# Performance work log

Hardware: AMD Instinct MI355X
Metric: run time of the kernel (lower is better)

Reference implementation:

```python
import jax, jax.numpy as jnp
import numpy as np

HEADS = 32
K_TOP = 512  # top-k tokens gathered from KV


def conv3d(x, w, b=None, pad=0, groups=1):
    # x: [B,C,D,H,W], w: [O, I/groups, kd,kh,kw]
    out = jax.lax.conv_general_dilated(
        x, w, window_strides=(1, 1, 1), padding=[(pad, pad)] * 3,
        dimension_numbers=("NCDHW", "OIDHW", "NCDHW"), feature_group_count=groups)
    if b is not None:
        out = out + b[None, :, None, None, None]
    return out


def setup_inputs() -> dict:
    key = jax.random.key(0)
    ks = jax.random.split(key, 10)
    B, C, D, H, W = 2, 256, 16, 16, 16
    p = lambda i, shape: (jax.random.normal(ks[i], shape, jnp.float32) * 0.02)
    return {
        "x_kv": jax.random.normal(ks[0], (B, C, D, H, W), jnp.float32),
        "x_q": jax.random.normal(ks[1], (B, C, D, H, W), jnp.float32),
        "w_spa": p(2, (1, 2, 7, 7, 7)),            # SpatialAttention conv, no bias
        "w_kv": p(3, (C, 2 * C)), "b_kv": jnp.zeros((2 * C,), jnp.float32),
        "w_q": p(4, (C, C)), "b_q": jnp.zeros((C,), jnp.float32),
        "w_proj": p(5, (C, C)), "b_proj": jnp.zeros((C,), jnp.float32),
        "w_dw": p(6, (C, 1, 3, 3, 3)), "b_dw": jnp.zeros((C,), jnp.float32),  # depthwise 3x3x3
        "w_pw": p(7, (C, C, 1, 1, 1)), "b_pw": jnp.zeros((C,), jnp.float32),  # pointwise 1x1x1
    }


def reference(x_kv, x_q, w_spa, w_kv, b_kv, w_q, b_q, w_proj, b_proj,
              w_dw, b_dw, w_pw, b_pw):
    B, C, D, H, W = x_kv.shape
    N = D * H * W
    hd = C // HEADS
    scale = hd ** -0.5

    # SpatialAttention: channel mean/max -> conv(2->1, k=7, pad=3) -> sigmoid
    avg = jnp.mean(x_kv, axis=1, keepdims=True)
    mx = jnp.max(x_kv, axis=1, keepdims=True)
    spa = jax.nn.sigmoid(conv3d(jnp.concatenate([avg, mx], axis=1), w_spa, None, pad=3))
    scores = spa.reshape(B, N)                      # [B, N]
    _, idx = jax.lax.top_k(scores, K_TOP)           # [B, K] (descending, like torch.topk)

    # Full K/V projection over all N tokens (as in original), then gather top-k
    xkv_t = x_kv.reshape(B, C, N).transpose(0, 2, 1)        # [B, N, C]
    kv = xkv_t @ w_kv + b_kv                                 # [B, N, 2C]
    k_full, v_full = kv[..., :C], kv[..., C:]
    k_g = jnp.take_along_axis(k_full, idx[:, :, None], axis=1)  # [B, K, C]
    v_g = jnp.take_along_axis(v_full, idx[:, :, None], axis=1)
    k_g = k_g.reshape(B, K_TOP, HEADS, hd).transpose(0, 2, 1, 3)  # [B, h, K, d]
    v_g = v_g.reshape(B, K_TOP, HEADS, hd).transpose(0, 2, 1, 3)

    # Queries over all Nq tokens
    xq_t = x_q.reshape(B, C, N).transpose(0, 2, 1)           # [B, N, C]
    q = (xq_t @ w_q + b_q).reshape(B, N, HEADS, hd).transpose(0, 2, 1, 3)  # [B, h, N, d]

    attn = jax.nn.softmax(jnp.einsum('bhnd,bhkd->bhnk', q, k_g) * scale, axis=-1)
    out = jnp.einsum('bhnk,bhkd->bhnd', attn, v_g)           # [B, h, N, d]
    out = out.transpose(0, 2, 1, 3).reshape(B, N, C)
    out = out @ w_proj + b_proj
    out = out.transpose(0, 2, 1).reshape(B, C, D, H, W)

    # DWconv residual on full (ungathered) V
    v_vol = v_full.transpose(0, 2, 1).reshape(B, C, D, H, W)
    res = conv3d(conv3d(v_vol, w_dw, b_dw, pad=1, groups=C), w_pw, b_pw)
    return out + res
```

## Files before the change

### kernel.cpp

```cpp
#include <hip/hip_runtime.h>
#include <hip/hip_bf16.h>

typedef short bf16x8 __attribute__((ext_vector_type(8)));
typedef float f32x4 __attribute__((ext_vector_type(4)));

constexpr int CN = 256, NV = 4096, KTOP = 512;

static __device__ __forceinline__ unsigned short f2bf(float f) {
  __hip_bfloat16 h = __float2bfloat16(f);
  return *(unsigned short*)&h;
}
static __device__ __forceinline__ unsigned pack2(float a, float b) {
  return (unsigned)f2bf(a) | ((unsigned)f2bf(b) << 16);
}
static __device__ __forceinline__ float bf2f(unsigned short u) {
  return __uint_as_float(((unsigned)u) << 16);
}
static __device__ __forceinline__ unsigned packtrunc(float a, float b) {
  return (__float_as_uint(a) >> 16) | (__float_as_uint(b) & 0xFFFF0000u);
}

__global__ void __launch_bounds__(256) k_tcast2(const float* __restrict__ srcA,
                                                const float* __restrict__ srcB,
                                                unsigned short* __restrict__ dstA,
                                                unsigned short* __restrict__ dstB,
                                                float* __restrict__ avgmx) {
  __shared__ float tile[64 * 65];
  int z = blockIdx.z;
  int t = threadIdx.x;
  if (z == 4) {
    __shared__ float ssum[256], smax[256];
    int blk = blockIdx.y * 64 + blockIdx.x;
    int b = blk >> 7, n0 = (blk & 127) * 32;
    int cg = t >> 5, nl = t & 31;
    int n = n0 + nl;
    const float* p = srcA + (size_t)b * CN * NV + (size_t)cg * 32 * NV + n;
    float s = 0.f, m = -1e30f;
    for (int i = 0; i < 32; ++i) {
      float v = p[(size_t)i * NV];
      s += v; m = fmaxf(m, v);
    }
    ssum[t] = s; smax[t] = m;
    __syncthreads();
    if (cg == 0) {
      for (int g = 1; g < 8; ++g) { s += ssum[g * 32 + nl]; m = fmaxf(m, smax[g * 32 + nl]); }
      avgmx[(b * 2 + 0) * NV + n] = s * (1.0f / 256.0f);
      avgmx[(b * 2 + 1) * NV + n] = m;
    }
    return;
  }
  int b = z & 1;
  const float* s = (z < 2 ? srcA : srcB) + (size_t)b * CN * NV;
  unsigned short* d = (z < 2 ? dstA : dstB) + (size_t)b * NV * 256;
  int c0 = blockIdx.y * 64, n0 = blockIdx.x * 64;
  for (int i = 0; i < 16; ++i) {
    int id = i * 256 + t, c = id >> 6, n = id & 63;
    tile[c * 65 + n] = s[(size_t)(c0 + c) * NV + n0 + n];
  }
  __syncthreads();
  int n = t & 63, part = t >> 6;
  unsigned w[8];
#pragma unroll
  for (int k = 0; k < 8; ++k)
    w[k] = pack2(tile[(part * 16 + 2 * k) * 65 + n], tile[(part * 16 + 2 * k + 1) * 65 + n]);
  uint4* p = (uint4*)&d[(size_t)(n0 + n) * 256 + c0 + part * 16];
  p[0] = make_uint4(w[0], w[1], w[2], w[3]);
  p[1] = make_uint4(w[4], w[5], w[6], w[7]);
}

__global__ void __launch_bounds__(256) k_wprep(const float* __restrict__ wkv,
                                               const float* __restrict__ wq,
                                               const float* __restrict__ wproj,
                                               const float* __restrict__ wpw,
                                               unsigned short* __restrict__ wv_t,
                                               unsigned short* __restrict__ wq_t,
                                               unsigned short* __restrict__ wcat,
                                               unsigned short* __restrict__ wk_t) {
  __shared__ float tile[64 * 65];
  int role = blockIdx.z;
  int j0 = blockIdx.x * 64, c0 = blockIdx.y * 64;
  int t = threadIdx.x;
  if (role == 3) {
    int j = t >> 2, part = t & 3;
    const float* s = &wpw[(size_t)(j0 + j) * 256 + c0 + part * 16];
    unsigned w[8];
#pragma unroll
    for (int k = 0; k < 8; ++k) w[k] = pack2(s[2 * k], s[2 * k + 1]);
    uint4* p = (uint4*)&wcat[(size_t)(j0 + j) * 512 + 256 + c0 + part * 16];
    p[0] = make_uint4(w[0], w[1], w[2], w[3]);
    p[1] = make_uint4(w[4], w[5], w[6], w[7]);
    return;
  }
  const float* src; int srcLD, srcOff; unsigned short* dst; int dstLD;
  if (role == 0)      { src = wkv;   srcLD = 512; srcOff = 256; dst = wv_t; dstLD = 256; }
  else if (role == 1) { src = wq;    srcLD = 256; srcOff = 0;   dst = wq_t; dstLD = 256; }
  else if (role == 4) { src = wkv;   srcLD = 512; srcOff = 0;   dst = wk_t; dstLD = 256; }
  else                { src = wproj; srcLD = 256; srcOff = 0;   dst = wcat; dstLD = 512; }
  for (int i = 0; i < 16; ++i) {
    int id = i * 256 + t, c = id >> 6, j = id & 63;
    tile[c * 65 + j] = src[(size_t)(c0 + c) * srcLD + srcOff + j0 + j];
  }
  __syncthreads();
  int j = t & 63, part = t >> 6;
  unsigned w[8];
#pragma unroll
  for (int k = 0; k < 8; ++k)
    w[k] = pack2(tile[(part * 16 + 2 * k) * 65 + j], tile[(part * 16 + 2 * k + 1) * 65 + j]);
  uint4* p = (uint4*)&dst[(size_t)(j0 + j) * dstLD + c0 + part * 16];
  p[0] = make_uint4(w[0], w[1], w[2], w[3]);
  p[1] = make_uint4(w[4], w[5], w[6], w[7]);
}

__global__ void __launch_bounds__(256) k_spa(const float* __restrict__ avgmx,
                                             const float* __restrict__ wspa,
                                             float* __restrict__ scores) {
  __shared__ float vol[2 * 4096];
  __shared__ float ws[686];
  int b = blockIdx.x >> 5, chunk = blockIdx.x & 31;
  int tid = threadIdx.x;
  for (int t = tid; t < 8192; t += 256) vol[t] = avgmx[b * 8192 + t];
  for (int t = tid; t < 686; t += 256) ws[t] = wspa[t];
  __syncthreads();
  int ci = tid & 1;
  int n = chunk * 128 + (tid >> 1);
  int d = n >> 8, h = (n >> 4) & 15, w = n & 15;
  const float* vb = vol + ci * 4096;
  const float* wb = ws + ci * 343;
  float acc = 0.f;
  for (int kd = 0; kd < 7; ++kd) {
    int zd = d - 3 + kd; if ((unsigned)zd >= 16u) continue;
    for (int kh = 0; kh < 7; ++kh) {
      int zh = h - 3 + kh; if ((unsigned)zh >= 16u) continue;
      const float* row = vb + zd * 256 + zh * 16;
      const float* wr = wb + kd * 49 + kh * 7;
#pragma unroll
      for (int kw = 0; kw < 7; ++kw) {
        int zw = w - 3 + kw;
        if ((unsigned)zw < 16u) acc += row[zw] * wr[kw];
      }
    }
  }
  acc += __shfl_xor(acc, 1);
  if (ci == 0) scores[b * NV + n] = 1.0f / (1.0f + expf(-acc));
}

__global__ void __launch_bounds__(1024) k_topk(const float* __restrict__ scores,
                                               int* __restrict__ idx) {
  __shared__ unsigned sv[4096];
  __shared__ int sB;
  __shared__ unsigned sSub, scnt;
  __shared__ unsigned hist[256];
  __shared__ int wsum[16];
  int b = blockIdx.x, tid = threadIdx.x;
  for (int t = tid; t < 4096; t += 1024) sv[t] = __float_as_uint(scores[b * NV + t]);
  if (tid == 0) scnt = 0;
  unsigned prefix = 0;
  int r = 512;
  for (int shift = 24; shift >= 0; shift -= 8) {
    if (tid < 256) hist[tid] = 0;
    __syncthreads();
    unsigned maskhi = (shift == 24) ? 0u : (0xFFFFFFFFu << (shift + 8));
    for (int i = 0; i < 4; ++i) {
      unsigned v = sv[tid + i * 1024];
      if ((v & maskhi) == prefix) atomicAdd(&hist[(v >> shift) & 255], 1u);
    }
    __syncthreads();
    if (tid < 64) {
      int lane = tid;
      unsigned h0 = hist[lane * 4 + 0], h1 = hist[lane * 4 + 1];
      unsigned h2 = hist[lane * 4 + 2], h3 = hist[lane * 4 + 3];
      unsigned s = h0 + h1 + h2 + h3;
      for (int off = 1; off < 64; off <<= 1) {
        unsigned y = __shfl_down(s, off);
        if (lane + off < 64) s += y;
      }
      unsigned tail = __shfl_down(s, 1);
      if (lane == 63) tail = 0;
      unsigned s3 = tail + h3, s2 = s3 + h2, s1 = s2 + h1, s0 = s1 + h0;
      unsigned sx[5] = {s0, s1, s2, s3, tail};
#pragma unroll
      for (int i = 0; i < 4; ++i)
        if (sx[i] >= (unsigned)r && sx[i + 1] < (unsigned)r) { sB = lane * 4 + i; sSub = sx[i + 1]; }
    }
    __syncthreads();
    prefix |= ((unsigned)sB) << shift;
    r -= (int)sSub;
    __syncthreads();
  }
  unsigned vstar = prefix;
  for (int i = 0; i < 4; ++i) {
    int t = tid * 4 + i;
    if (sv[t] > vstar) { unsigned p = atomicAdd(&scnt, 1u); idx[b * KTOP + p] = t; }
  }
  __syncthreads();
  int base = (int)scnt;
  int loc = 0;
  for (int i = 0; i < 4; ++i) loc += (sv[tid * 4 + i] == vstar);
  int lane = tid & 63, w = tid >> 6;
  int x = loc;
  for (int off = 1; off < 64; off <<= 1) {
    int y = __shfl_up(x, off);
    if (lane >= off) x += y;
  }
  if (lane == 63) wsum[w] = x;
  __syncthreads();
  int wbase = 0;
  for (int i = 0; i < w; ++i) wbase += wsum[i];
  int excl = wbase + x - loc;
  for (int i = 0; i < 4; ++i) {
    int t = tid * 4 + i;
    if (sv[t] == vstar) {
      if (excl < r) idx[b * KTOP + base + excl] = t;
      ++excl;
    }
  }
}

__global__ void __launch_bounds__(256) k_qv(const unsigned short* __restrict__ xkv_t,
                                            const unsigned short* __restrict__ xq_t,
                                            const unsigned short* __restrict__ wv_t,
                                            const unsigned short* __restrict__ wq_t,
                                            const float* __restrict__ bkv,
                                            const float* __restrict__ bq,
                                            unsigned short* __restrict__ v_nc,
                                            unsigned short* __restrict__ qh) {
  __shared__ unsigned short Als[128 * 40];
  __shared__ unsigned short Bls[128 * 40];
  int role = blockIdx.z;
  int b = role & 1;
  bool isQ = role >= 2;
  const unsigned short* A = isQ ? wq_t : wv_t;
  const unsigned short* B = (isQ ? xq_t : xkv_t) + (size_t)b * NV * 256;
  const float* bias = isQ ? bq : (bkv + 256);
  int n0 = blockIdx.x * 128, j0 = blockIdx.y * 128;
  int t = threadIdx.x;
  int wave = t >> 6, lane = t & 63;
  int l15 = lane & 15, q = lane >> 4, q8 = q * 8;
  int wj = (wave >> 1) * 64, wn = (wave & 1) * 64;
  f32x4 acc[4][4] = {};
  int ar = t >> 1, ah = t & 1;
  for (int c0 = 0; c0 < 256; c0 += 32) {
    __syncthreads();
    {
      const unsigned short* sa = &A[(size_t)(j0 + ar) * 256 + c0 + ah * 16];
      *(uint4*)&Als[ar * 40 + ah * 16]     = *(const uint4*)&sa[0];
      *(uint4*)&Als[ar * 40 + ah * 16 + 8] = *(const uint4*)&sa[8];
      const unsigned short* sb = &B[(size_t)(n0 + ar) * 256 + c0 + ah * 16];
      *(uint4*)&Bls[ar * 40 + ah * 16]     = *(const uint4*)&sb[0];
      *(uint4*)&Bls[ar * 40 + ah * 16 + 8] = *(const uint4*)&sb[8];
    }
    __syncthreads();
    bf16x8 af[4], bf[4];
#pragma unroll
    for (int mt = 0; mt < 4; ++mt)
      af[mt] = *(const bf16x8*)&Als[(wj + mt * 16 + l15) * 40 + q8];
#pragma unroll
    for (int nt = 0; nt < 4; ++nt)
      bf[nt] = *(const bf16x8*)&Bls[(wn + nt * 16 + l15) * 40 + q8];
#pragma unroll
    for (int mt = 0; mt < 4; ++mt)
#pragma unroll
      for (int nt = 0; nt < 4; ++nt)
        acc[mt][nt] = __builtin_amdgcn_mfma_f32_16x16x32_bf16(af[mt], bf[nt], acc[mt][nt], 0, 0, 0);
  }
#pragma unroll
  for (int mt = 0; mt < 4; ++mt) {
    int jb = j0 + wj + mt * 16 + q * 4;
    float4 b4 = *(const float4*)&bias[jb];
#pragma unroll
    for (int nt = 0; nt < 4; ++nt) {
      int n = n0 + wn + nt * 16 + l15;
      float v0 = acc[mt][nt][0] + b4.x;
      float v1 = acc[mt][nt][1] + b4.y;
      float v2 = acc[mt][nt][2] + b4.z;
      float v3 = acc[mt][nt][3] + b4.w;
      uint2 pk = make_uint2(pack2(v0, v1), pack2(v2, v3));
      if (isQ) {
        int h = jb >> 3, d0 = jb & 7;
        *(uint2*)&qh[((size_t)(b * 32 + h) * NV + n) * 8 + d0] = pk;
      } else {
        *(uint2*)&v_nc[((size_t)b * NV + n) * 256 + jb] = pk;
      }
    }
  }
}

__global__ void __launch_bounds__(256) k_kgvt(const unsigned short* __restrict__ xkv_t,
                                              const unsigned short* __restrict__ wk_t,
                                              const float* __restrict__ bkv,
                                              const int* __restrict__ map,
                                              const unsigned short* __restrict__ v_nc,
                                              unsigned short* __restrict__ kg,
                                              unsigned short* __restrict__ vt) {
  int b = blockIdx.z;
  int bx = blockIdx.x;
  int t = threadIdx.x;
  if (bx >= 128) {
    int h = bx - 128;
    int bh = b * 32 + h;
    unsigned short* dst = vt + (size_t)bh * 16 * 512;
    for (int i = t; i < 512; i += 256) dst[8 * 512 + i] = 0x3F80;
    for (int i = t; i < 512 * 7; i += 256) dst[9 * 512 + i] = 0;
    const int* ib = map + b * KTOP;
    for (int kk = t; kk < 512; kk += 256) {
      uint4 v = *(const uint4*)&v_nc[((size_t)b * NV + ib[kk]) * 256 + h * 8];
      unsigned short tmp[8];
      *(uint4*)tmp = v;
      int kc = kk >> 5, ka = kk & 31;
      int s = (ka < 16) ? ((ka >> 2) * 8 + (ka & 3))
                        : (((ka - 16) >> 2) * 8 + (ka & 3) + 4);
      int col = kc * 32 + s;
#pragma unroll
      for (int d = 0; d < 8; ++d) dst[d * 512 + col] = tmp[d];
    }
    return;
  }
  const float kscale = 0.35355339059327373f * 1.4426950408889634f;
  int wave = t >> 6, lane = t & 63;
  int l15 = lane & 15, quad = lane >> 4;
  int tile_id = bx * 4 + wave;
  int kt = tile_id & 31, jt = tile_id >> 5;
  int m0 = kt * 16, j0 = jt * 16;
  int nrow = map[b * KTOP + m0 + l15];
  const unsigned short* Arow = wk_t + (size_t)(j0 + l15) * 256 + quad * 8;
  const unsigned short* Brow = xkv_t + (size_t)b * NV * 256 + (size_t)nrow * 256 + quad * 8;
  f32x4 acc = {0.f, 0.f, 0.f, 0.f};
#pragma unroll
  for (int s = 0; s < 8; ++s) {
    bf16x8 af = *(const bf16x8*)&Arow[s * 32];
    bf16x8 bf = *(const bf16x8*)&Brow[s * 32];
    acc = __builtin_amdgcn_mfma_f32_16x16x32_bf16(af, bf, acc, 0, 0, 0);
  }
  int h = (j0 >> 3) + (quad >> 1), d0b = (quad & 1) * 4;
  int jb = j0 + quad * 4;
  float4 b4 = *(const float4*)&bkv[jb];
  int m = m0 + l15;
  float v0 = (acc[0] + b4.x) * kscale;
  float v1 = (acc[1] + b4.y) * kscale;
  float v2 = (acc[2] + b4.z) * kscale;
  float v3 = (acc[3] + b4.w) * kscale;
  *(uint2*)&kg[((size_t)(b * 32 + h) * KTOP + m) * 8 + d0b] =
      make_uint2(pack2(v0, v1), pack2(v2, v3));
}

__global__ void __launch_bounds__(256) k_fattn(const unsigned short* __restrict__ qh,
                                               const unsigned short* __restrict__ kg,
                                               const unsigned short* __restrict__ vt,
                                               unsigned short* __restrict__ aoydw) {
  int bh = blockIdx.x;
  int b = bh >> 5, h = bh & 31;
  int t = threadIdx.x, wave = t >> 6, lane = t & 63;
  int l15 = lane & 15, quad = lane >> 4;
  int n0 = blockIdx.y * 128 + wave * 32;
  bf16x8 q0 = {}, q1 = {};
  if (quad == 0) {
    q0 = *(const bf16x8*)&qh[((size_t)bh * NV + n0 + l15) * 8];
    q1 = *(const bf16x8*)&qh[((size_t)bh * NV + n0 + 16 + l15) * 8];
  }
  const unsigned short* kbase = kg + (size_t)bh * KTOP * 8;
  const unsigned short* vbase = vt + (size_t)bh * 16 * 512;
  f32x4 acc0 = {0.f, 0.f, 0.f, 0.f}, acc1 = {0.f, 0.f, 0.f, 0.f};
  bf16x8 kA0 = {}, kA1 = {};
  if (quad == 0) {
    kA0 = *(const bf16x8*)&kbase[(size_t)l15 * 8];
    kA1 = *(const bf16x8*)&kbase[(size_t)(16 + l15) * 8];
  }
  for (int kc = 0; kc < 16; ++kc) {
    bf16x8 nA0 = {}, nA1 = {};
    if (quad == 0 && kc < 15) {
      nA0 = *(const bf16x8*)&kbase[(size_t)(kc * 32 + 32 + l15) * 8];
      nA1 = *(const bf16x8*)&kbase[(size_t)(kc * 32 + 48 + l15) * 8];
    }
    bf16x8 bV = *(const bf16x8*)&vbase[(size_t)l15 * 512 + kc * 32 + quad * 8];
    f32x4 z = {0.f, 0.f, 0.f, 0.f};
    f32x4 s00 = __builtin_amdgcn_mfma_f32_16x16x32_bf16(kA0, q0, z, 0, 0, 0);
    f32x4 s01 = __builtin_amdgcn_mfma_f32_16x16x32_bf16(kA1, q0, z, 0, 0, 0);
    f32x4 s10 = __builtin_amdgcn_mfma_f32_16x16x32_bf16(kA0, q1, z, 0, 0, 0);
    f32x4 s11 = __builtin_amdgcn_mfma_f32_16x16x32_bf16(kA1, q1, z, 0, 0, 0);
    uint4 P0, P1;
    P0.x = packtrunc(__builtin_amdgcn_exp2f(s00[0]), __builtin_amdgcn_exp2f(s00[1]));
    P0.y = packtrunc(__builtin_amdgcn_exp2f(s00[2]), __builtin_amdgcn_exp2f(s00[3]));
    P0.z = packtrunc(__builtin_amdgcn_exp2f(s01[0]), __builtin_amdgcn_exp2f(s01[1]));
    P0.w = packtrunc(__builtin_amdgcn_exp2f(s01[2]), __builtin_amdgcn_exp2f(s01[3]));
    P1.x = packtrunc(__builtin_amdgcn_exp2f(s10[0]), __builtin_amdgcn_exp2f(s10[1]));
    P1.y = packtrunc(__builtin_amdgcn_exp2f(s10[2]), __builtin_amdgcn_exp2f(s10[3]));
    P1.z = packtrunc(__builtin_amdgcn_exp2f(s11[0]), __builtin_amdgcn_exp2f(s11[1]));
    P1.w = packtrunc(__builtin_amdgcn_exp2f(s11[2]), __builtin_amdgcn_exp2f(s11[3]));
    acc0 = __builtin_amdgcn_mfma_f32_16x16x32_bf16(*(bf16x8*)&P0, bV, acc0, 0, 0, 0);
    acc1 = __builtin_amdgcn_mfma_f32_16x16x32_bf16(*(bf16x8*)&P1, bV, acc1, 0, 0, 0);
    kA0 = nA0; kA1 = nA1;
  }
#pragma unroll
  for (int tq = 0; tq < 2; ++tq) {
    f32x4 a = tq ? acc1 : acc0;
#pragma unroll
    for (int r = 0; r < 4; ++r) {
      float se = __shfl(a[r], quad * 16 + 8);
      float o = a[r] * (1.0f / se);
      if (l15 < 8) {
        int n = n0 + tq * 16 + quad * 4 + r;
        aoydw[((size_t)b * NV + n) * 512 + h * 8 + l15] = f2bf(o);
      }
    }
  }
}

__global__ void __launch_bounds__(256) k_dw(const unsigned short* __restrict__ v_nc,
                                            const float* __restrict__ wdw,
                                            const float* __restrict__ bdw,
                                            unsigned short* __restrict__ aoydw) {
  int c = threadIdx.x;
  int b = blockIdx.y;
  float wr[27];
#pragma unroll
  for (int i = 0; i < 27; ++i) wr[i] = wdw[c * 27 + i];
  float bias = bdw[c];
  const unsigned short* src = v_nc + (size_t)b * NV * 256 + c;
  unsigned short* dst = aoydw + (size_t)b * NV * 512 + 256 + c;
  int n = blockIdx.x * 4;
  int d = n >> 8, h = (n >> 4) & 15, w = n & 15;
  float a0 = bias, a1 = bias, a2 = bias, a3 = bias;
#pragma unroll
  for (int kd = 0; kd < 3; ++kd) {
    int zd = d - 1 + kd; bool okd = (unsigned)zd < 16u;
#pragma unroll
    for (int kh = 0; kh < 3; ++kh) {
      int zh = h - 1 + kh; bool okh = okd && ((unsigned)zh < 16u);
      int rowb = zd * 256 + zh * 16;
      float v[6];
#pragma unroll
      for (int i = 0; i < 6; ++i) {
        int zw = w - 1 + i;
        bool ok = okh && ((unsigned)zw < 16u);
        v[i] = ok ? bf2f(src[(size_t)(rowb + zw) * 256]) : 0.f;
      }
      const float* wp = &wr[kd * 9 + kh * 3];
      a0 = fmaf(v[0], wp[0], fmaf(v[1], wp[1], fmaf(v[2], wp[2], a0)));
      a1 = fmaf(v[1], wp[0], fmaf(v[2], wp[1], fmaf(v[3], wp[2], a1)));
      a2 = fmaf(v[2], wp[0], fmaf(v[3], wp[1], fmaf(v[4], wp[2], a2)));
      a3 = fmaf(v[3], wp[0], fmaf(v[4], wp[1], fmaf(v[5], wp[2], a3)));
    }
  }
  dst[(size_t)(n + 0) * 512] = f2bf(a0);
  dst[(size_t)(n + 1) * 512] = f2bf(a1);
  dst[(size_t)(n + 2) * 512] = f2bf(a2);
  dst[(size_t)(n + 3) * 512] = f2bf(a3);
}

__global__ void __launch_bounds__(256) k_final(const unsigned short* __restrict__ aoydw,
                                               const unsigned short* __restrict__ wcat,
                                               const float* __restrict__ bproj,
                                               const float* __restrict__ bpw,
                                               float* __restrict__ out) {
  __shared__ unsigned short Als[64 * 40];
  __shared__ unsigned short Bls[128 * 40];
  int n0 = blockIdx.x * 64, j0 = blockIdx.y * 128, b = blockIdx.z;
  int t = threadIdx.x;
  int wave = t >> 6, lane = t & 63;
  int l15 = lane & 15, q = lane >> 4, q8 = q * 8;
  int wn = (wave >> 1) * 32, wjj = (wave & 1) * 64;
  f32x4 acc[2][4] = {};
  const unsigned short* Abase = aoydw + (size_t)b * NV * 512;
  int ar = t >> 2, aq = t & 3;
  int br = t >> 1, bhh = t & 1;
  for (int c0 = 0; c0 < 512; c0 += 32) {
    __syncthreads();
    *(uint4*)&Als[ar * 40 + aq * 8] =
        *(const uint4*)&Abase[(size_t)(n0 + ar) * 512 + c0 + aq * 8];
    const unsigned short* sb = &wcat[(size_t)(j0 + br) * 512 + c0 + bhh * 16];
    *(uint4*)&Bls[br * 40 + bhh * 16]     = *(const uint4*)&sb[0];
    *(uint4*)&Bls[br * 40 + bhh * 16 + 8] = *(const uint4*)&sb[8];
    __syncthreads();
    bf16x8 af[2], bf[4];
#pragma unroll
    for (int mt = 0; mt < 2; ++mt)
      af[mt] = *(const bf16x8*)&Als[(wn + mt * 16 + l15) * 40 + q8];
#pragma unroll
    for (int nt = 0; nt < 4; ++nt)
      bf[nt] = *(const bf16x8*)&Bls[(wjj + nt * 16 + l15) * 40 + q8];
#pragma unroll
    for (int mt = 0; mt < 2; ++mt)
#pragma unroll
      for (int nt = 0; nt < 4; ++nt)
        acc[mt][nt] = __builtin_amdgcn_mfma_f32_16x16x32_bf16(af[mt], bf[nt], acc[mt][nt], 0, 0, 0);
  }
#pragma unroll
  for (int nt = 0; nt < 4; ++nt) {
    int j = j0 + wjj + nt * 16 + l15;
    float bl = bproj[j] + bpw[j];
#pragma unroll
    for (int mt = 0; mt < 2; ++mt) {
      int n = n0 + wn + mt * 16 + q * 4;
      float4 r = make_float4(acc[mt][nt][0] + bl, acc[mt][nt][1] + bl,
                             acc[mt][nt][2] + bl, acc[mt][nt][3] + bl);
      *(float4*)&out[(size_t)(b * 256 + j) * NV + n] = r;
    }
  }
}

extern "C" void kernel_launch(void* const* d_in, const int* in_sizes, int n_in,
                              void* d_out, int out_size, void* d_ws, size_t ws_size,
                              hipStream_t stream) {
  const float* x_kv   = (const float*)d_in[0];
  const float* x_q    = (const float*)d_in[1];
  const float* w_spa  = (const float*)d_in[2];
  const float* w_kv   = (const float*)d_in[3];
  const float* b_kv   = (const float*)d_in[4];
  const float* w_q    = (const float*)d_in[5];
  const float* b_q    = (const float*)d_in[6];
  const float* w_proj = (const float*)d_in[7];
  const float* b_proj = (const float*)d_in[8];
  const float* w_dw   = (const float*)d_in[9];
  const float* b_dw   = (const float*)d_in[10];
  const float* w_pw   = (const float*)d_in[11];
  const float* b_pw   = (const float*)d_in[12];
  float* out = (float*)d_out;

  const size_t MB = 1024 * 1024;
  char* ws = (char*)d_ws;
  unsigned short* xkv_t = (unsigned short*)(ws);
  unsigned short* xq_t  = (unsigned short*)(ws + 4 * MB);
  unsigned short* v_nc  = (unsigned short*)(ws + 8 * MB);
  unsigned short* qh    = (unsigned short*)(ws + 12 * MB);
  unsigned short* aoydw = (unsigned short*)(ws + 16 * MB);
  unsigned short* kg    = (unsigned short*)(ws + 24 * MB);
  unsigned short* vt    = (unsigned short*)(ws + 24 * MB + 512 * 1024);
  unsigned short* wv_t  = (unsigned short*)(ws + 26 * MB);
  unsigned short* wq_t  = (unsigned short*)(ws + 26 * MB + 131072);
  unsigned short* wcat  = (unsigned short*)(ws + 26 * MB + 262144);
  unsigned short* wk_t  = (unsigned short*)(ws + 26 * MB + 524288);
  float*          avgmx = (float*)(ws + 27 * MB);
  float*          scores= (float*)(ws + 27 * MB + 65536);
  int*            idx   = (int*)  (ws + 27 * MB + 98304);

  k_tcast2<<<dim3(64, 4, 5), 256, 0, stream>>>(x_kv, x_q, xkv_t, xq_t, avgmx);
  k_wprep<<<dim3(4, 4, 5), 256, 0, stream>>>(w_kv, w_q, w_proj, w_pw, wv_t, wq_t, wcat, wk_t);
  k_spa<<<64, 256, 0, stream>>>(avgmx, w_spa, scores);
  k_topk<<<2, 1024, 0, stream>>>(scores, idx);
  k_qv<<<dim3(32, 2, 4), 256, 0, stream>>>(xkv_t, xq_t, wv_t, wq_t, b_kv, b_q, v_nc, qh);
  k_kgvt<<<dim3(160, 1, 2), 256, 0, stream>>>(xkv_t, wk_t, b_kv, idx, v_nc, kg, vt);
  k_fattn<<<dim3(64, 32), 256, 0, stream>>>(qh, kg, vt, aoydw);
  k_dw<<<dim3(1024, 2), 256, 0, stream>>>(v_nc, w_dw, b_dw, aoydw);
  k_final<<<dim3(64, 2, 2), 256, 0, stream>>>(aoydw, wcat, b_proj, b_pw, out);
}
```

Before: 205.2 us.

## Merge independent kernels into three multi-role launches to cut launch count

Independent stages now share launches through blockIdx.z roles. Weight prep runs inside the transpose/cast kernel, the spatial conv inside the Q/V projection kernel, and top-k inside the depthwise conv kernel. This takes the launch count from nine to six and lets small serial kernels overlap with larger ones. In exchange, the stage1 grid carries many early-exit blocks, and the depthwise conv now runs as 1024-thread blocks that share a launch with the single-block-per-batch top-k, which may reduce occupancy.

After: 188.1 us. 1.09x faster.

```diff
diff --git a/kernel.cpp b/kernel.cpp
--- a/kernel.cpp
+++ b/kernel.cpp
@@ -20,11 +20,19 @@
   return (__float_as_uint(a) >> 16) | (__float_as_uint(b) & 0xFFFF0000u);
 }
 
-__global__ void __launch_bounds__(256) k_tcast2(const float* __restrict__ srcA,
-                                                const float* __restrict__ srcB,
-                                                unsigned short* __restrict__ dstA,
-                                                unsigned short* __restrict__ dstB,
-                                                float* __restrict__ avgmx) {
+__global__ void __launch_bounds__(256) k_stage1(const float* __restrict__ xkv,
+                                                const float* __restrict__ xq,
+                                                const float* __restrict__ wkv,
+                                                const float* __restrict__ wq,
+                                                const float* __restrict__ wproj,
+                                                const float* __restrict__ wpw,
+                                                unsigned short* __restrict__ xkv_t,
+                                                unsigned short* __restrict__ xq_t,
+                                                float* __restrict__ avgmx,
+                                                unsigned short* __restrict__ wv_t,
+                                                unsigned short* __restrict__ wq_t,
+                                                unsigned short* __restrict__ wcat,
+                                                unsigned short* __restrict__ wk_t) {
   __shared__ float tile[64 * 65];
   int z = blockIdx.z;
   int t = threadIdx.x;
@@ -34,7 +42,7 @@
     int b = blk >> 7, n0 = (blk & 127) * 32;
     int cg = t >> 5, nl = t & 31;
     int n = n0 + nl;
-    const float* p = srcA + (size_t)b * CN * NV + (size_t)cg * 32 * NV + n;
+    const float* p = xkv + (size_t)b * CN * NV + (size_t)cg * 32 * NV + n;
     float s = 0.f, m = -1e30f;
     for (int i = 0; i < 32; ++i) {
       float v = p[(size_t)i * NV];
@@ -49,9 +57,44 @@
     }
     return;
   }
+  if (z >= 5) {
+    if (blockIdx.x >= 4 || blockIdx.y >= 4) return;
+    int role = z - 5;
+    int j0 = blockIdx.x * 64, c0 = blockIdx.y * 64;
+    if (role == 3) {
+      int j = t >> 2, part = t & 3;
+      const float* s = &wpw[(size_t)(j0 + j) * 256 + c0 + part * 16];
+      unsigned w[8];
+#pragma unroll
+      for (int k = 0; k < 8; ++k) w[k] = pack2(s[2 * k], s[2 * k + 1]);
+      uint4* p = (uint4*)&wcat[(size_t)(j0 + j) * 512 + 256 + c0 + part * 16];
+      p[0] = make_uint4(w[0], w[1], w[2], w[3]);
+      p[1] = make_uint4(w[4], w[5], w[6], w[7]);
+      return;
+    }
+    const float* src; int srcLD, srcOff; unsigned short* dst; int dstLD;
+    if (role == 0)      { src = wkv;   srcLD = 512; srcOff = 256; dst = wv_t; dstLD = 256; }
+    else if (role == 1) { src = wq;    srcLD = 256; srcOff = 0;   dst = wq_t; dstLD = 256; }
+    else if (role == 4) { src = wkv;   srcLD = 512; srcOff = 0;   dst = wk_t; dstLD = 256; }
+    else                { src = wproj; srcLD = 256; srcOff = 0;   dst = wcat; dstLD = 512; }
+    for (int i = 0; i < 16; ++i) {
+      int id = i * 256 + t, c = id >> 6, j = id & 63;
+      tile[c * 65 + j] = src[(size_t)(c0 + c) * srcLD + srcOff + j0 + j];
+    }
+    __syncthreads();
+    int j = t & 63, part = t >> 6;
+    unsigned w[8];
+#pragma unroll
+    for (int k = 0; k < 8; ++k)
+      w[k] = pack2(tile[(part * 16 + 2 * k) * 65 + j], tile[(part * 16 + 2 * k + 1) * 65 + j]);
+    uint4* p = (uint4*)&dst[(size_t)(j0 + j) * dstLD + c0 + part * 16];
+    p[0] = make_uint4(w[0], w[1], w[2], w[3]);
+    p[1] = make_uint4(w[4], w[5], w[6], w[7]);
+    return;
+  }
   int b = z & 1;
-  const float* s = (z < 2 ? srcA : srcB) + (size_t)b * CN * NV;
-  unsigned short* d = (z < 2 ? dstA : dstB) + (size_t)b * NV * 256;
+  const float* s = (z < 2 ? xkv : xq) + (size_t)b * CN * NV;
+  unsigned short* d = (z < 2 ? xkv_t : xq_t) + (size_t)b * NV * 256;
   int c0 = blockIdx.y * 64, n0 = blockIdx.x * 64;
   for (int i = 0; i < 16; ++i) {
     int id = i * 256 + t, c = id >> 6, n = id & 63;
@@ -68,172 +111,60 @@
   p[1] = make_uint4(w[4], w[5], w[6], w[7]);
 }
 
-__global__ void __launch_bounds__(256) k_wprep(const float* __restrict__ wkv,
-                                               const float* __restrict__ wq,
-                                               const float* __restrict__ wproj,
-                                               const float* __restrict__ wpw,
-                                               unsigned short* __restrict__ wv_t,
-                                               unsigned short* __restrict__ wq_t,
-                                               unsigned short* __restrict__ wcat,
-                                               unsigned short* __restrict__ wk_t) {
-  __shared__ float tile[64 * 65];
-  int role = blockIdx.z;
-  int j0 = blockIdx.x * 64, c0 = blockIdx.y * 64;
+__global__ void __launch_bounds__(256) k_stage2(const unsigned short* __restrict__ xkv_t,
+                                                const unsigned short* __restrict__ xq_t,
+                                                const unsigned short* __restrict__ wv_t,
+                                                const unsigned short* __restrict__ wq_t,
+                                                const float* __restrict__ bkv,
+                                                const float* __restrict__ bq,
+                                                const float* __restrict__ avgmx,
+                                                const float* __restrict__ wspa,
+                                                unsigned short* __restrict__ v_nc,
+                                                unsigned short* __restrict__ qh,
+                                                float* __restrict__ scores) {
+  __shared__ alignas(16) char smem[35520];
+  int z = blockIdx.z;
   int t = threadIdx.x;
-  if (role == 3) {
-    int j = t >> 2, part = t & 3;
-    const float* s = &wpw[(size_t)(j0 + j) * 256 + c0 + part * 16];
-    unsigned w[8];
-#pragma unroll
-    for (int k = 0; k < 8; ++k) w[k] = pack2(s[2 * k], s[2 * k + 1]);
-    uint4* p = (uint4*)&wcat[(size_t)(j0 + j) * 512 + 256 + c0 + part * 16];
-    p[0] = make_uint4(w[0], w[1], w[2], w[3]);
-    p[1] = make_uint4(w[4], w[5], w[6], w[7]);
+  if (z == 4) {
+    float* vol = (float*)smem;
+    float* ws = (float*)(smem + 32768);
+    int id = blockIdx.y * 32 + blockIdx.x;
+    int b = id >> 5, chunk = id & 31;
+    for (int i = t; i < 8192; i += 256) vol[i] = avgmx[b * 8192 + i];
+    for (int i = t; i < 686; i += 256) ws[i] = wspa[i];
+    __syncthreads();
+    int ci = t & 1;
+    int n = chunk * 128 + (t >> 1);
+    int d = n >> 8, h = (n >> 4) & 15, w = n & 15;
+    const float* vb = vol + ci * 4096;
+    const float* wb = ws + ci * 343;
+    float acc = 0.f;
+    for (int kd = 0; kd < 7; ++kd) {
+      int zd = d - 3 + kd; if ((unsigned)zd >= 16u) continue;
+      for (int kh = 0; kh < 7; ++kh) {
+        int zh = h - 3 + kh; if ((unsigned)zh >= 16u) continue;
+        const float* row = vb + zd * 256 + zh * 16;
+        const float* wr = wb + kd * 49 + kh * 7;
+#pragma unroll
+        for (int kw = 0; kw < 7; ++kw) {
+          int zw = w - 3 + kw;
+          if ((unsigned)zw < 16u) acc += row[zw] * wr[kw];
+        }
+      }
+    }
+    acc += __shfl_xor(acc, 1);
+    if (ci == 0) scores[b * NV + n] = 1.0f / (1.0f + expf(-acc));
     return;
   }
-  const float* src; int srcLD, srcOff; unsigned short* dst; int dstLD;
-  if (role == 0)      { src = wkv;   srcLD = 512; srcOff = 256; dst = wv_t; dstLD = 256; }
-  else if (role == 1) { src = wq;    srcLD = 256; srcOff = 0;   dst = wq_t; dstLD = 256; }
-  else if (role == 4) { src = wkv;   srcLD = 512; srcOff = 0;   dst = wk_t; dstLD = 256; }
-  else                { src = wproj; srcLD = 256; srcOff = 0;   dst = wcat; dstLD = 512; }
-  for (int i = 0; i < 16; ++i) {
-    int id = i * 256 + t, c = id >> 6, j = id & 63;
-    tile[c * 65 + j] = src[(size_t)(c0 + c) * srcLD + srcOff + j0 + j];
-  }
-  __syncthreads();
-  int j = t & 63, part = t >> 6;
-  unsigned w[8];
-#pragma unroll
-  for (int k = 0; k < 8; ++k)
-    w[k] = pack2(tile[(part * 16 + 2 * k) * 65 + j], tile[(part * 16 + 2 * k + 1) * 65 + j]);
-  uint4* p = (uint4*)&dst[(size_t)(j0 + j) * dstLD + c0 + part * 16];
-  p[0] = make_uint4(w[0], w[1], w[2], w[3]);
-  p[1] = make_uint4(w[4], w[5], w[6], w[7]);
-}
-
-__global__ void __launch_bounds__(256) k_spa(const float* __restrict__ avgmx,
-                                             const float* __restrict__ wspa,
-                                             float* __restrict__ scores) {
-  __shared__ float vol[2 * 4096];
-  __shared__ float ws[686];
-  int b = blockIdx.x >> 5, chunk = blockIdx.x & 31;
-  int tid = threadIdx.x;
-  for (int t = tid; t < 8192; t += 256) vol[t] = avgmx[b * 8192 + t];
-  for (int t = tid; t < 686; t += 256) ws[t] = wspa[t];
-  __syncthreads();
-  int ci = tid & 1;
-  int n = chunk * 128 + (tid >> 1);
-  int d = n >> 8, h = (n >> 4) & 15, w = n & 15;
-  const float* vb = vol + ci * 4096;
-  const float* wb = ws + ci * 343;
-  float acc = 0.f;
-  for (int kd = 0; kd < 7; ++kd) {
-    int zd = d - 3 + kd; if ((unsigned)zd >= 16u) continue;
-    for (int kh = 0; kh < 7; ++kh) {
-      int zh = h - 3 + kh; if ((unsigned)zh >= 16u) continue;
-      const float* row = vb + zd * 256 + zh * 16;
-      const float* wr = wb + kd * 49 + kh * 7;
-#pragma unroll
-      for (int kw = 0; kw < 7; ++kw) {
-        int zw = w - 3 + kw;
-        if ((unsigned)zw < 16u) acc += row[zw] * wr[kw];
-      }
-    }
-  }
-  acc += __shfl_xor(acc, 1);
-  if (ci == 0) scores[b * NV + n] = 1.0f / (1.0f + expf(-acc));
-}
-
-__global__ void __launch_bounds__(1024) k_topk(const float* __restrict__ scores,
-                                               int* __restrict__ idx) {
-  __shared__ unsigned sv[4096];
-  __shared__ int sB;
-  __shared__ unsigned sSub, scnt;
-  __shared__ unsigned hist[256];
-  __shared__ int wsum[16];
-  int b = blockIdx.x, tid = threadIdx.x;
-  for (int t = tid; t < 4096; t += 1024) sv[t] = __float_as_uint(scores[b * NV + t]);
-  if (tid == 0) scnt = 0;
-  unsigned prefix = 0;
-  int r = 512;
-  for (int shift = 24; shift >= 0; shift -= 8) {
-    if (tid < 256) hist[tid] = 0;
-    __syncthreads();
-    unsigned maskhi = (shift == 24) ? 0u : (0xFFFFFFFFu << (shift + 8));
-    for (int i = 0; i < 4; ++i) {
-      unsigned v = sv[tid + i * 1024];
-      if ((v & maskhi) == prefix) atomicAdd(&hist[(v >> shift) & 255], 1u);
-    }
-    __syncthreads();
-    if (tid < 64) {
-      int lane = tid;
-      unsigned h0 = hist[lane * 4 + 0], h1 = hist[lane * 4 + 1];
-      unsigned h2 = hist[lane * 4 + 2], h3 = hist[lane * 4 + 3];
-      unsigned s = h0 + h1 + h2 + h3;
-      for (int off = 1; off < 64; off <<= 1) {
-        unsigned y = __shfl_down(s, off);
-        if (lane + off < 64) s += y;
-      }
-      unsigned tail = __shfl_down(s, 1);
-      if (lane == 63) tail = 0;
-      unsigned s3 = tail + h3, s2 = s3 + h2, s1 = s2 + h1, s0 = s1 + h0;
-      unsigned sx[5] = {s0, s1, s2, s3, tail};
-#pragma unroll
-      for (int i = 0; i < 4; ++i)
-        if (sx[i] >= (unsigned)r && sx[i + 1] < (unsigned)r) { sB = lane * 4 + i; sSub = sx[i + 1]; }
-    }
-    __syncthreads();
-    prefix |= ((unsigned)sB) << shift;
-    r -= (int)sSub;
-    __syncthreads();
-  }
-  unsigned vstar = prefix;
-  for (int i = 0; i < 4; ++i) {
-    int t = tid * 4 + i;
-    if (sv[t] > vstar) { unsigned p = atomicAdd(&scnt, 1u); idx[b * KTOP + p] = t; }
-  }
-  __syncthreads();
-  int base = (int)scnt;
-  int loc = 0;
-  for (int i = 0; i < 4; ++i) loc += (sv[tid * 4 + i] == vstar);
-  int lane = tid & 63, w = tid >> 6;
-  int x = loc;
-  for (int off = 1; off < 64; off <<= 1) {
-    int y = __shfl_up(x, off);
-    if (lane >= off) x += y;
-  }
-  if (lane == 63) wsum[w] = x;
-  __syncthreads();
-  int wbase = 0;
-  for (int i = 0; i < w; ++i) wbase += wsum[i];
-  int excl = wbase + x - loc;
-  for (int i = 0; i < 4; ++i) {
-    int t = tid * 4 + i;
-    if (sv[t] == vstar) {
-      if (excl < r) idx[b * KTOP + base + excl] = t;
-      ++excl;
-    }
-  }
-}
-
-__global__ void __launch_bounds__(256) k_qv(const unsigned short* __restrict__ xkv_t,
-                                            const unsigned short* __restrict__ xq_t,
-                                            const unsigned short* __restrict__ wv_t,
-                                            const unsigned short* __restrict__ wq_t,
-                                            const float* __restrict__ bkv,
-                                            const float* __restrict__ bq,
-                                            unsigned short* __restrict__ v_nc,
-                                            unsigned short* __restrict__ qh) {
-  __shared__ unsigned short Als[128 * 40];
-  __shared__ unsigned short Bls[128 * 40];
-  int role = blockIdx.z;
+  unsigned short* Als = (unsigned short*)smem;
+  unsigned short* Bls = Als + 128 * 40;
+  int role = z;
   int b = role & 1;
   bool isQ = role >= 2;
   const unsigned short* A = isQ ? wq_t : wv_t;
   const unsigned short* B = (isQ ? xq_t : xkv_t) + (size_t)b * NV * 256;
   const float* bias = isQ ? bq : (bkv + 256);
   int n0 = blockIdx.x * 128, j0 = blockIdx.y * 128;
-  int t = threadIdx.x;
   int wave = t >> 6, lane = t & 63;
   int l15 = lane & 15, q = lane >> 4, q8 = q * 8;
   int wj = (wave >> 1) * 64, wn = (wave & 1) * 64;
@@ -283,6 +214,122 @@
       }
     }
   }
+}
+
+__global__ void __launch_bounds__(1024) k_stage3(const float* __restrict__ scores,
+                                                 int* __restrict__ idx,
+                                                 const unsigned short* __restrict__ v_nc,
+                                                 const float* __restrict__ wdw,
+                                                 const float* __restrict__ bdw,
+                                                 unsigned short* __restrict__ aoydw) {
+  int b = blockIdx.z;
+  int bx = blockIdx.x;
+  int tid = threadIdx.x;
+  if (bx == 256) {
+    __shared__ unsigned sv[4096];
+    __shared__ int sB;
+    __shared__ unsigned sSub, scnt;
+    __shared__ unsigned hist[256];
+    __shared__ int wsum[16];
+    for (int t = tid; t < 4096; t += 1024) sv[t] = __float_as_uint(scores[b * NV + t]);
+    if (tid == 0) scnt = 0;
+    unsigned prefix = 0;
+    int r = 512;
+    for (int shift = 24; shift >= 0; shift -= 8) {
+      if (tid < 256) hist[tid] = 0;
+      __syncthreads();
+      unsigned maskhi = (shift == 24) ? 0u : (0xFFFFFFFFu << (shift + 8));
+      for (int i = 0; i < 4; ++i) {
+        unsigned v = sv[tid + i * 1024];
+        if ((v & maskhi) == prefix) atomicAdd(&hist[(v >> shift) & 255], 1u);
+      }
+      __syncthreads();
+      if (tid < 64) {
+        int lane = tid;
+        unsigned h0 = hist[lane * 4 + 0], h1 = hist[lane * 4 + 1];
+        unsigned h2 = hist[lane * 4 + 2], h3 = hist[lane * 4 + 3];
+        unsigned s = h0 + h1 + h2 + h3;
+        for (int off = 1; off < 64; off <<= 1) {
+          unsigned y = __shfl_down(s, off);
+          if (lane + off < 64) s += y;
+        }
+        unsigned tail = __shfl_down(s, 1);
+        if (lane == 63) tail = 0;
+        unsigned s3 = tail + h3, s2 = s3 + h2, s1 = s2 + h1, s0 = s1 + h0;
+        unsigned sx[5] = {s0, s1, s2, s3, tail};
+#pragma unroll
+        for (int i = 0; i < 4; ++i)
+          if (sx[i] >= (unsigned)r && sx[i + 1] < (unsigned)r) { sB = lane * 4 + i; sSub = sx[i + 1]; }
+      }
+      __syncthreads();
+      prefix |= ((unsigned)sB) << shift;
+      r -= (int)sSub;
+      __syncthreads();
+    }
+    unsigned vstar = prefix;
+    for (int i = 0; i < 4; ++i) {
+      int t = tid * 4 + i;
+      if (sv[t] > vstar) { unsigned p = atomicAdd(&scnt, 1u); idx[b * KTOP + p] = t; }
+    }
+    __syncthreads();
+    int base = (int)scnt;
+    int loc = 0;
+    for (int i = 0; i < 4; ++i) loc += (sv[tid * 4 + i] == vstar);
+    int lane = tid & 63, w = tid >> 6;
+    int x = loc;
+    for (int off = 1; off < 64; off <<= 1) {
+      int y = __shfl_up(x, off);
+      if (lane >= off) x += y;
+    }
+    if (lane == 63) wsum[w] = x;
+    __syncthreads();
+    int wbase = 0;
+    for (int i = 0; i < w; ++i) wbase += wsum[i];
+    int excl = wbase + x - loc;
+    for (int i = 0; i < 4; ++i) {
+      int t = tid * 4 + i;
+      if (sv[t] == vstar) {
+        if (excl < r) idx[b * KTOP + base + excl] = t;
+        ++excl;
+      }
+    }
+    return;
+  }
+  int c = tid & 255;
+  float wr[27];
+#pragma unroll
+  for (int i = 0; i < 27; ++i) wr[i] = wdw[c * 27 + i];
+  float bias = bdw[c];
+  const unsigned short* src = v_nc + (size_t)b * NV * 256 + c;
+  unsigned short* dst = aoydw + (size_t)b * NV * 512 + 256 + c;
+  int n = bx * 16 + (tid >> 8) * 4;
+  int d = n >> 8, h = (n >> 4) & 15, w = n & 15;
+  float a0 = bias, a1 = bias, a2 = bias, a3 = bias;
+#pragma unroll
+  for (int kd = 0; kd < 3; ++kd) {
+    int zd = d - 1 + kd; bool okd = (unsigned)zd < 16u;
+#pragma unroll
+    for (int kh = 0; kh < 3; ++kh) {
+      int zh = h - 1 + kh; bool okh = okd && ((unsigned)zh < 16u);
+      int rowb = zd * 256 + zh * 16;
+      float v[6];
+#pragma unroll
+      for (int i = 0; i < 6; ++i) {
+        int zw = w - 1 + i;
+        bool ok = okh && ((unsigned)zw < 16u);
+        v[i] = ok ? bf2f(src[(size_t)(rowb + zw) * 256]) : 0.f;
+      }
+      const float* wp = &wr[kd * 9 + kh * 3];
+      a0 = fmaf(v[0], wp[0], fmaf(v[1], wp[1], fmaf(v[2], wp[2], a0)));
+      a1 = fmaf(v[1], wp[0], fmaf(v[2], wp[1], fmaf(v[3], wp[2], a1)));
+      a2 = fmaf(v[2], wp[0], fmaf(v[3], wp[1], fmaf(v[4], wp[2], a2)));
+      a3 = fmaf(v[3], wp[0], fmaf(v[4], wp[1], fmaf(v[5], wp[2], a3)));
+    }
+  }
+  dst[(size_t)(n + 0) * 512] = f2bf(a0);
+  dst[(size_t)(n + 1) * 512] = f2bf(a1);
+  dst[(size_t)(n + 2) * 512] = f2bf(a2);
+  dst[(size_t)(n + 3) * 512] = f2bf(a3);
 }
 
 __global__ void __launch_bounds__(256) k_kgvt(const unsigned short* __restrict__ xkv_t,
@@ -405,48 +452,6 @@
   }
 }
 
-__global__ void __launch_bounds__(256) k_dw(const unsigned short* __restrict__ v_nc,
-                                            const float* __restrict__ wdw,
-                                            const float* __restrict__ bdw,
-                                            unsigned short* __restrict__ aoydw) {
-  int c = threadIdx.x;
-  int b = blockIdx.y;
-  float wr[27];
-#pragma unroll
-  for (int i = 0; i < 27; ++i) wr[i] = wdw[c * 27 + i];
-  float bias = bdw[c];
-  const unsigned short* src = v_nc + (size_t)b * NV * 256 + c;
-  unsigned short* dst = aoydw + (size_t)b * NV * 512 + 256 + c;
-  int n = blockIdx.x * 4;
-  int d = n >> 8, h = (n >> 4) & 15, w = n & 15;
-  float a0 = bias, a1 = bias, a2 = bias, a3 = bias;
-#pragma unroll
-  for (int kd = 0; kd < 3; ++kd) {
-    int zd = d - 1 + kd; bool okd = (unsigned)zd < 16u;
-#pragma unroll
-    for (int kh = 0; kh < 3; ++kh) {
-      int zh = h - 1 + kh; bool okh = okd && ((unsigned)zh < 16u);
-      int rowb = zd * 256 + zh * 16;
-      float v[6];
-#pragma unroll
-      for (int i = 0; i < 6; ++i) {
-        int zw = w - 1 + i;
-        bool ok = okh && ((unsigned)zw < 16u);
-        v[i] = ok ? bf2f(src[(size_t)(rowb + zw) * 256]) : 0.f;
-      }
-      const float* wp = &wr[kd * 9 + kh * 3];
-      a0 = fmaf(v[0], wp[0], fmaf(v[1], wp[1], fmaf(v[2], wp[2], a0)));
-      a1 = fmaf(v[1], wp[0], fmaf(v[2], wp[1], fmaf(v[3], wp[2], a1)));
-      a2 = fmaf(v[2], wp[0], fmaf(v[3], wp[1], fmaf(v[4], wp[2], a2)));
-      a3 = fmaf(v[3], wp[0], fmaf(v[4], wp[1], fmaf(v[5], wp[2], a3)));
-    }
-  }
-  dst[(size_t)(n + 0) * 512] = f2bf(a0);
-  dst[(size_t)(n + 1) * 512] = f2bf(a1);
-  dst[(size_t)(n + 2) * 512] = f2bf(a2);
-  dst[(size_t)(n + 3) * 512] = f2bf(a3);
-}
-
 __global__ void __launch_bounds__(256) k_final(const unsigned short* __restrict__ aoydw,
                                                const unsigned short* __restrict__ wcat,
                                                const float* __restrict__ bproj,
@@ -533,13 +538,12 @@
   float*          scores= (float*)(ws + 27 * MB + 65536);
   int*            idx   = (int*)  (ws + 27 * MB + 98304);
 
-  k_tcast2<<<dim3(64, 4, 5), 256, 0, stream>>>(x_kv, x_q, xkv_t, xq_t, avgmx);
-  k_wprep<<<dim3(4, 4, 5), 256, 0, stream>>>(w_kv, w_q, w_proj, w_pw, wv_t, wq_t, wcat, wk_t);
-  k_spa<<<64, 256, 0, stream>>>(avgmx, w_spa, scores);
-  k_topk<<<2, 1024, 0, stream>>>(scores, idx);
-  k_qv<<<dim3(32, 2, 4), 256, 0, stream>>>(xkv_t, xq_t, wv_t, wq_t, b_kv, b_q, v_nc, qh);
+  k_stage1<<<dim3(64, 4, 10), 256, 0, stream>>>(x_kv, x_q, w_kv, w_q, w_proj, w_pw,
+                                                xkv_t, xq_t, avgmx, wv_t, wq_t, wcat, wk_t);
+  k_stage2<<<dim3(32, 2, 5), 256, 0, stream>>>(xkv_t, xq_t, wv_t, wq_t, b_kv, b_q,
+                                               avgmx, w_spa, v_nc, qh, scores);
+  k_stage3<<<dim3(257, 1, 2), 1024, 0, stream>>>(scores, idx, v_nc, w_dw, b_dw, aoydw);
   k_kgvt<<<dim3(160, 1, 2), 256, 0, stream>>>(xkv_t, wk_t, b_kv, idx, v_nc, kg, vt);
   k_fattn<<<dim3(64, 32), 256, 0, stream>>>(qh, kg, vt, aoydw);
-  k_dw<<<dim3(1024, 2), 256, 0, stream>>>(v_nc, w_dw, b_dw, aoydw);
   k_final<<<dim3(64, 2, 2), 256, 0, stream>>>(aoydw, wcat, b_proj, b_pw, out);
 }
```
